# Performance work log

Measured on AMD Instinct MI355X. Metric: run time of the kernel, lower is better.

Reference implementation:

```python
import jax, jax.numpy as jnp
import numpy as np
import math

B, L, C, H = 2, 2048, 768, 12
D = C // H
MAX_SCALE_MUL = math.log(100.0)


def setup_inputs() -> dict:
    key = jax.random.key(0)
    ks = jax.random.split(key, 8)
    std = 0.02
    x = jax.random.normal(ks[0], (B, L, C), dtype=jnp.float32)
    attn_bias = jax.random.normal(ks[1], (1, 1, L, L), dtype=jnp.float32)
    W_qkv = jax.random.normal(ks[2], (3 * C, C), dtype=jnp.float32) * std
    b_qkv = jnp.zeros((3 * C,), dtype=jnp.float32)
    # attn_l2_norm=True: learned per-head log-scale, init log(4)
    scale_mul_log = jnp.full((1, H, 1, 1), math.log(4.0), dtype=jnp.float32)
    W_proj = jax.random.normal(ks[3], (C, C), dtype=jnp.float32) * std
    b_proj = jnp.zeros((C,), dtype=jnp.float32)
    return {"x": x, "attn_bias": attn_bias, "W_qkv": W_qkv, "b_qkv": b_qkv,
            "scale_mul_log": scale_mul_log, "W_proj": W_proj, "b_proj": b_proj}


def _l2norm(t):
    # matches F.normalize(dim=-1, eps=1e-12)
    n = jnp.sqrt(jnp.sum(t * t, axis=-1, keepdims=True))
    return t / jnp.maximum(n, 1e-12)


def reference(x, attn_bias, W_qkv, b_qkv, scale_mul_log, W_proj, b_proj):
    Bx, Lx, Cx = x.shape
    qkv = (x @ W_qkv.T + b_qkv).reshape(Bx, Lx, 3, H, D)
    # -> [3, B, H, L, D]
    qkv = jnp.transpose(qkv, (2, 0, 3, 1, 4))
    q, k, v = qkv[0], qkv[1], qkv[2]
    scale_mul = jnp.exp(jnp.minimum(scale_mul_log, MAX_SCALE_MUL))  # [1,H,1,1]
    q = _l2norm(q) * scale_mul
    k = _l2norm(k)
    # scale = 1 in the l2-norm branch
    attn = jnp.einsum('bhqd,bhkd->bhqk', q, k) + attn_bias
    attn = jax.nn.softmax(attn, axis=-1)
    oup = jnp.einsum('bhqk,bhkd->bhqd', attn, v)          # [B,H,L,D]
    oup = jnp.transpose(oup, (0, 2, 1, 3)).reshape(Bx, Lx, Cx)
    return oup @ W_proj.T + b_proj
```

## Files before the change

kernel.cpp:

```cpp
#include <hip/hip_runtime.h>
#include <math.h>

#define B_ 2
#define L_ 2048
#define C_ 768
#define H_ 12
#define D_ 64
#define M_ (B_ * L_)
#define MAXLOG 4.605170185988091f

typedef __bf16 bf16;
typedef __bf16 bf16x4 __attribute__((ext_vector_type(4)));
typedef __bf16 bf16x8 __attribute__((ext_vector_type(8)));
typedef float  f32x4  __attribute__((ext_vector_type(4)));
typedef short  s16x4  __attribute__((ext_vector_type(4)));

#define SZ_  ((size_t)B_ * H_ * L_ * D_)
#define MC_  ((size_t)M_ * C_)
#define WQ_  ((size_t)3 * C_ * C_)
#define WP_  ((size_t)C_ * C_)

static __device__ __forceinline__ f32x4 mfma16(bf16x4 a, bf16x4 b, f32x4 c) {
#if __has_builtin(__builtin_amdgcn_mfma_f32_16x16x16_bf16)
    return __builtin_amdgcn_mfma_f32_16x16x16_bf16(a, b, c, 0, 0, 0);
#elif __has_builtin(__builtin_amdgcn_mfma_f32_16x16x16bf16_1k)
    return __builtin_amdgcn_mfma_f32_16x16x16bf16_1k(*(s16x4*)&a, *(s16x4*)&b, c, 0, 0, 0);
#else
    f32x4 d;
    asm("v_mfma_f32_16x16x16_bf16 %0, %1, %2, %3" : "=v"(d) : "v"(a), "v"(b), "v"(c));
    return d;
#endif
}

static __device__ __forceinline__ void stage16(const bf16* gsrc, void* ldst) {
#if __has_builtin(__builtin_amdgcn_global_load_lds)
    __builtin_amdgcn_global_load_lds(
        (const __attribute__((address_space(1))) unsigned int*)gsrc,
        (__attribute__((address_space(3))) unsigned int*)ldst, 16, 0, 0);
#else
    *(bf16x8*)ldst = *(const bf16x8*)gsrc;
#endif
}

__global__ __launch_bounds__(256) void prep(
    const float4* __restrict__ x, const float4* __restrict__ Wq,
    const float4* __restrict__ Wp,
    bf16* __restrict__ xb, bf16* __restrict__ wqb,
    bf16* __restrict__ Wh, bf16* __restrict__ Wl)
{
    const int X4 = (int)(MC_ / 4);
    const int W4 = (int)(WQ_ / 4);
    const int S4 = (int)(WP_ / 4);
    const int total = X4 + W4 + S4;

    const int i0 = blockIdx.x * 256 + threadIdx.x;
    const int stride = gridDim.x * 256;
    for (int i = i0; i < total; i += stride) {
        if (i < X4) {
            const float4 v = x[i];
            bf16x4 o; o[0]=(bf16)v.x; o[1]=(bf16)v.y; o[2]=(bf16)v.z; o[3]=(bf16)v.w;
            *(bf16x4*)&xb[(size_t)i * 4] = o;
        } else if (i < X4 + W4) {
            const int j = i - X4;
            const float4 v = Wq[j];
            bf16x4 o; o[0]=(bf16)v.x; o[1]=(bf16)v.y; o[2]=(bf16)v.z; o[3]=(bf16)v.w;
            *(bf16x4*)&wqb[(size_t)j * 4] = o;
        } else {
            const int j = i - X4 - W4;
            const float4 v = Wp[j];
            bf16x4 h, l;
            h[0]=(bf16)v.x; l[0]=(bf16)(v.x-(float)h[0]);
            h[1]=(bf16)v.y; l[1]=(bf16)(v.y-(float)h[1]);
            h[2]=(bf16)v.z; l[2]=(bf16)(v.z-(float)h[2]);
            h[3]=(bf16)v.w; l[3]=(bf16)(v.w-(float)h[3]);
            *(bf16x4*)&Wh[(size_t)j * 4] = h;
            *(bf16x4*)&Wl[(size_t)j * 4] = l;
        }
    }
}

__global__ __launch_bounds__(256) void qkv_mfma(
    const bf16* __restrict__ A, const bf16* __restrict__ W,
    const float* __restrict__ bias, const float* __restrict__ sml,
    bf16* __restrict__ qb, bf16* __restrict__ kb, bf16* __restrict__ vtb)
{
    __shared__ __align__(16) bf16 As[128][64];
    __shared__ __align__(16) bf16 Bs[64][64];

    const int t    = threadIdx.x;
    const int w    = t >> 6;
    const int lane = t & 63;
    const int quad = lane >> 4;
    const int c    = lane & 15;
    const int m0   = blockIdx.x * 128;
    const int n0   = blockIdx.y * 64;

    const int sr = t >> 3;
    const int sc = t & 7;
    const int sx = sc ^ (sr & 7);

    f32x4 acc[2][4];
    #pragma unroll
    for (int mt = 0; mt < 2; ++mt)
        #pragma unroll
        for (int nt = 0; nt < 4; ++nt) acc[mt][nt] = (f32x4){0.f,0.f,0.f,0.f};

    for (int kt = 0; kt < C_; kt += 64) {
        __syncthreads();
        #pragma unroll
        for (int p = 0; p < 4; ++p)
            stage16(&A[(size_t)(m0 + 32 * p + sr) * C_ + kt + 8 * sx],
                    (char*)&As[0][0] + (p * 256 + t) * 16);
        #pragma unroll
        for (int p = 0; p < 2; ++p)
            stage16(&W[(size_t)(n0 + 32 * p + sr) * C_ + kt + 8 * sx],
                    (char*)&Bs[0][0] + (p * 256 + t) * 16);
        __syncthreads();

        #pragma unroll
        for (int ks = 0; ks < 2; ++ks) {
            const int rchunk = ((4 * ks + quad) ^ (c & 7)) * 16;
            #pragma unroll
            for (int mt = 0; mt < 2; ++mt) {
                const bf16x8 a = *(const bf16x8*)((const char*)&As[0][0]
                                 + (size_t)(w * 32 + mt * 16 + c) * 128 + rchunk);
                #pragma unroll
                for (int nt = 0; nt < 4; ++nt) {
                    const bf16x8 b = *(const bf16x8*)((const char*)&Bs[0][0]
                                     + (size_t)(nt * 16 + c) * 128 + rchunk);
                    acc[mt][nt] = __builtin_amdgcn_mfma_f32_16x16x32_bf16(a, b, acc[mt][nt], 0, 0, 0);
                }
            }
        }
    }

    const int three = blockIdx.y / H_;
    const int h     = blockIdx.y % H_;
    const int bidx  = m0 >> 11;
    const int l0    = (m0 & (L_ - 1)) + w * 32;

    if (three < 2) {
        bf16* dst = (three == 0) ? qb : kb;
        const float scale = (three == 0) ? expf(fminf(sml[h], MAXLOG)) : 1.0f;
        #pragma unroll
        for (int mt = 0; mt < 2; ++mt) {
            float val[4][4];
            float ss[4] = {0.f, 0.f, 0.f, 0.f};
            #pragma unroll
            for (int nt = 0; nt < 4; ++nt) {
                const float bb = bias[n0 + nt * 16 + c];
                #pragma unroll
                for (int reg = 0; reg < 4; ++reg) {
                    const float v = acc[mt][nt][reg] + bb;
                    val[nt][reg] = v;
                    ss[reg] += v * v;
                }
            }
            #pragma unroll
            for (int reg = 0; reg < 4; ++reg) {
                float s = ss[reg];
                #pragma unroll
                for (int off = 1; off < 16; off <<= 1) s += __shfl_xor(s, off, 16);
                const float inv = scale / fmaxf(sqrtf(s), 1e-12f);
                const int l = l0 + mt * 16 + quad * 4 + reg;
                #pragma unroll
                for (int nt = 0; nt < 4; ++nt)
                    dst[((size_t)(bidx * H_ + h) * L_ + l) * D_ + nt * 16 + c] =
                        (bf16)(val[nt][reg] * inv);
            }
        }
    } else {
        #pragma unroll
        for (int mt = 0; mt < 2; ++mt)
            #pragma unroll
            for (int nt = 0; nt < 4; ++nt) {
                const int d = nt * 16 + c;
                const float bb = bias[n0 + d];
                const int l = l0 + mt * 16 + quad * 4;
                bf16x4 o;
                #pragma unroll
                for (int reg = 0; reg < 4; ++reg) o[reg] = (bf16)(acc[mt][nt][reg] + bb);
                *(bf16x4*)&vtb[((size_t)(bidx * H_ + h) * D_ + d) * L_ + l] = o;
            }
    }
}

__global__ __launch_bounds__(256, 3) void flash_mfma(
    const bf16* __restrict__ q, const bf16* __restrict__ k,
    const bf16* __restrict__ vt, const float* __restrict__ bias,
    const float* __restrict__ sml,
    bf16* __restrict__ aoh, bf16* __restrict__ aol)
{
    __shared__ __align__(16) bf16 Ks0 [64][72];
    __shared__ __align__(16) bf16 Ks1 [64][72];
    __shared__ __align__(16) bf16 Vts0[64][72];
    __shared__ __align__(16) bf16 Vts1[64][72];

    const int t    = threadIdx.x;
    const int w    = t >> 6;
    const int lane = t & 63;
    const int quad = lane >> 4;
    const int c    = lane & 15;
    const int q0   = blockIdx.x * 64;
    const int bh   = blockIdx.y;
    const int h    = bh % H_;
    const int b    = bh / H_;
    const size_t base  = (size_t)bh * L_ * D_;
    const size_t vbase = (size_t)bh * D_ * L_;
    const int qrow = q0 + w * 16 + c;

    const float FMAX = expf(fminf(sml[h], MAXLOG)) + 8.0f;

    bf16x8 qf[2];
    qf[0] = *(const bf16x8*)&q[base + (size_t)qrow * D_ + quad * 8];
    qf[1] = *(const bf16x8*)&q[base + (size_t)qrow * D_ + 32 + quad * 8];

    const int r0  = t >> 3,         c00 = (t & 7) * 8;
    const int r1  = (t + 256) >> 3, c01 = ((t + 256) & 7) * 8;

    const size_t brow = (size_t)qrow * L_ + 4 * quad;

    float l_acc = 0.f;
    f32x4 o[4];
    #pragma unroll
    for (int dt = 0; dt < 4; ++dt) o[dt] = (f32x4){0.f, 0.f, 0.f, 0.f};

    bf16x8 kreg[2], vreg[2];
    f32x4  bregA[4], bregB[4];

    kreg[0] = *(const bf16x8*)&k [base  + (size_t)r0 * D_ + c00];
    kreg[1] = *(const bf16x8*)&k [base  + (size_t)r1 * D_ + c01];
    vreg[0] = *(const bf16x8*)&vt[vbase + (size_t)r0 * L_ + c00];
    vreg[1] = *(const bf16x8*)&vt[vbase + (size_t)r1 * L_ + c01];
    #pragma unroll
    for (int s = 0; s < 4; ++s)
        bregA[s] = *(const f32x4*)&bias[brow + 16 * s];

    *(bf16x8*)&Ks0 [r0][c00] = kreg[0];
    *(bf16x8*)&Ks0 [r1][c01] = kreg[1];
    *(bf16x8*)&Vts0[r0][c00] = vreg[0];
    *(bf16x8*)&Vts0[r1][c01] = vreg[1];

    kreg[0] = *(const bf16x8*)&k [base  + (size_t)(64 + r0) * D_ + c00];
    kreg[1] = *(const bf16x8*)&k [base  + (size_t)(64 + r1) * D_ + c01];
    vreg[0] = *(const bf16x8*)&vt[vbase + (size_t)r0 * L_ + 64 + c00];
    vreg[1] = *(const bf16x8*)&vt[vbase + (size_t)r1 * L_ + 64 + c01];
    #pragma unroll
    for (int s = 0; s < 4; ++s)
        bregB[s] = *(const f32x4*)&bias[brow + 64 + 16 * s];
    __syncthreads();

#define FSTEP(KS_C, VT_C, KS_N, VT_N, BC, IT) do {                               \
    if ((IT) + 1 < 32) {                                                         \
        *(bf16x8*)&KS_N [r0][c00] = kreg[0];                                     \
        *(bf16x8*)&KS_N [r1][c01] = kreg[1];                                     \
        *(bf16x8*)&VT_N [r0][c00] = vreg[0];                                     \
        *(bf16x8*)&VT_N [r1][c01] = vreg[1];                                     \
    }                                                                            \
    f32x4 st[4];                                                                 \
    _Pragma("unroll") for (int s = 0; s < 4; ++s) st[s] = BC[s];                 \
    if ((IT) + 2 < 32) {                                                         \
        const int kp = ((IT) + 2) * 64;                                          \
        kreg[0] = *(const bf16x8*)&k [base  + (size_t)(kp + r0) * D_ + c00];     \
        kreg[1] = *(const bf16x8*)&k [base  + (size_t)(kp + r1) * D_ + c01];     \
        vreg[0] = *(const bf16x8*)&vt[vbase + (size_t)r0 * L_ + kp + c00];       \
        vreg[1] = *(const bf16x8*)&vt[vbase + (size_t)r1 * L_ + kp + c01];       \
        _Pragma("unroll") for (int s = 0; s < 4; ++s)                            \
            BC[s] = *(const f32x4*)&bias[brow + kp + 16 * s];                    \
    }                                                                            \
    _Pragma("unroll") for (int ks = 0; ks < 2; ++ks)                             \
        _Pragma("unroll") for (int s = 0; s < 4; ++s) {                          \
            const bf16x8 kf = *(const bf16x8*)&KS_C[s*16 + c][ks*32 + quad*8];   \
            st[s] = __builtin_amdgcn_mfma_f32_16x16x32_bf16(kf, qf[ks], st[s], 0, 0, 0); \
        }                                                                        \
    bf16x4 pf[4];                                                                \
    _Pragma("unroll") for (int s = 0; s < 4; ++s)                                \
        _Pragma("unroll") for (int r = 0; r < 4; ++r) {                          \
            const float pv = __expf(st[s][r] - FMAX);                            \
            l_acc += pv;                                                         \
            pf[s][r] = (bf16)pv;                                                 \
        }                                                                        \
    _Pragma("unroll") for (int s = 0; s < 4; ++s)                                \
        _Pragma("unroll") for (int dt = 0; dt < 4; ++dt) {                       \
            const bf16x4 vfr = *(const bf16x4*)&VT_C[dt*16 + c][16*s + 4*quad];  \
            o[dt] = mfma16(vfr, pf[s], o[dt]);                                   \
        }                                                                        \
    __syncthreads();                                                             \
} while (0)

    for (int it = 0; it < 32; it += 2) {
        FSTEP(Ks0, Vts0, Ks1, Vts1, bregA, it);
        FSTEP(Ks1, Vts1, Ks0, Vts0, bregB, it + 1);
    }
#undef FSTEP

    float rs = l_acc;
    rs += __shfl_xor(rs, 16);
    rs += __shfl_xor(rs, 32);
    const float linv = 1.0f / rs;

    const size_t obase = ((size_t)(b * L_ + qrow)) * C_ + h * 64;
    #pragma unroll
    for (int dt = 0; dt < 4; ++dt) {
        bf16x4 hv, lv;
        #pragma unroll
        for (int r = 0; r < 4; ++r) {
            const float v = o[dt][r] * linv;
            hv[r] = (bf16)v;
            lv[r] = (bf16)(v - (float)hv[r]);
        }
        *(bf16x4*)&aoh[obase + dt * 16 + 4 * quad] = hv;
        *(bf16x4*)&aol[obase + dt * 16 + 4 * quad] = lv;
    }
}

__global__ __launch_bounds__(256) void proj_mfma(
    const bf16* __restrict__ Ahg, const bf16* __restrict__ Alg,
    const bf16* __restrict__ Whg, const bf16* __restrict__ Wlg,
    const float* __restrict__ bias, float* __restrict__ outp)
{
    __shared__ __align__(16) bf16 Ah[64][64];
    __shared__ __align__(16) bf16 Al[64][64];
    __shared__ __align__(16) bf16 Bh[64][64];
    __shared__ __align__(16) bf16 Bl[64][64];

    const int t    = threadIdx.x;
    const int w    = t >> 6;
    const int lane = t & 63;
    const int quad = lane >> 4;
    const int c    = lane & 15;
    const int m0   = blockIdx.x * 64;
    const int n0   = blockIdx.y * 64;

    const int sr = t >> 3;
    const int sc = t & 7;
    const int sx = sc ^ (sr & 7);

    f32x4 acc[4];
    #pragma unroll
    for (int nt = 0; nt < 4; ++nt) acc[nt] = (f32x4){0.f,0.f,0.f,0.f};

    for (int kt = 0; kt < C_; kt += 64) {
        __syncthreads();
        #pragma unroll
        for (int p = 0; p < 2; ++p) {
            const size_t ga = (size_t)(m0 + 32 * p + sr) * C_ + kt + 8 * sx;
            const size_t gb = (size_t)(n0 + 32 * p + sr) * C_ + kt + 8 * sx;
            const int    lo = (p * 256 + t) * 16;
            stage16(&Ahg[ga], (char*)&Ah[0][0] + lo);
            stage16(&Alg[ga], (char*)&Al[0][0] + lo);
            stage16(&Whg[gb], (char*)&Bh[0][0] + lo);
            stage16(&Wlg[gb], (char*)&Bl[0][0] + lo);
        }
        __syncthreads();

        #pragma unroll
        for (int ks = 0; ks < 2; ++ks) {
            const int rchunk = ((4 * ks + quad) ^ (c & 7)) * 16;
            const bf16x8 ah = *(const bf16x8*)((const char*)&Ah[0][0]
                              + (size_t)(w * 16 + c) * 128 + rchunk);
            const bf16x8 al = *(const bf16x8*)((const char*)&Al[0][0]
                              + (size_t)(w * 16 + c) * 128 + rchunk);
            #pragma unroll
            for (int nt = 0; nt < 4; ++nt) {
                const bf16x8 bh = *(const bf16x8*)((const char*)&Bh[0][0]
                                  + (size_t)(nt * 16 + c) * 128 + rchunk);
                const bf16x8 bl = *(const bf16x8*)((const char*)&Bl[0][0]
                                  + (size_t)(nt * 16 + c) * 128 + rchunk);
                acc[nt] = __builtin_amdgcn_mfma_f32_16x16x32_bf16(ah, bh, acc[nt], 0, 0, 0);
                acc[nt] = __builtin_amdgcn_mfma_f32_16x16x32_bf16(ah, bl, acc[nt], 0, 0, 0);
                acc[nt] = __builtin_amdgcn_mfma_f32_16x16x32_bf16(al, bh, acc[nt], 0, 0, 0);
            }
        }
    }

    #pragma unroll
    for (int nt = 0; nt < 4; ++nt) {
        const int col = n0 + nt * 16 + c;
        const float bb = bias[col];
        #pragma unroll
        for (int reg = 0; reg < 4; ++reg) {
            const int row = m0 + w * 16 + quad * 4 + reg;
            outp[(size_t)row * C_ + col] = acc[nt][reg] + bb;
        }
    }
}

extern "C" void kernel_launch(void* const* d_in, const int* in_sizes, int n_in,
                              void* d_out, int out_size, void* d_ws, size_t ws_size,
                              hipStream_t stream)
{
    const float* x         = (const float*)d_in[0];
    const float* attn_bias = (const float*)d_in[1];
    const float* W_qkv     = (const float*)d_in[2];
    const float* b_qkv     = (const float*)d_in[3];
    const float* sml       = (const float*)d_in[4];
    const float* W_proj    = (const float*)d_in[5];
    const float* b_proj    = (const float*)d_in[6];
    float* out = (float*)d_out;

    bf16* qb  = (bf16*)d_ws;
    bf16* kb  = qb  + SZ_;
    bf16* vtb = kb  + SZ_;
    bf16* aoh = vtb + SZ_;
    bf16* aol = aoh + MC_;
    bf16* Wh  = aol + MC_;
    bf16* Wl  = Wh  + WP_;
    bf16* xb  = Wl  + WP_;
    bf16* wqb = xb  + MC_;

    prep<<<2048, 256, 0, stream>>>(
        (const float4*)x, (const float4*)W_qkv, (const float4*)W_proj,
        xb, wqb, Wh, Wl);

    qkv_mfma<<<dim3(M_ / 128, (3 * C_) / 64), 256, 0, stream>>>(
        xb, wqb, b_qkv, sml, qb, kb, vtb);

    flash_mfma<<<dim3(L_ / 64, B_ * H_), 256, 0, stream>>>(
        qb, kb, vtb, attn_bias, sml, aoh, aol);

    proj_mfma<<<dim3(M_ / 64, C_ / 64), 256, 0, stream>>>(
        aoh, aol, Wh, Wl, b_proj, out);
}
```

Before: 200.4 us.

## Split flash attention keys across wave pairs with 2x query reuse per wave

Reorganizes the flash attention block so each wave handles 32 query rows (two 16-row tiles sharing each K/V fragment load) and the four waves split the key range into two halves processed in parallel. K/V tiles become 32-key chunks per half, and the partial outputs and row sums of the two key-halves are merged through shared memory at the end. This is meant to halve LDS fragment reads per MFMA and improve MFMA density, at the cost of more accumulator registers, an extra LDS reduction buffer and a final sync.

```diff
diff --git a/kernel.cpp b/kernel.cpp
--- a/kernel.cpp
+++ b/kernel.cpp
@@ -191,126 +191,172 @@
     const float* __restrict__ sml,
     bf16* __restrict__ aoh, bf16* __restrict__ aol)
 {
-    __shared__ __align__(16) bf16 Ks0 [64][72];
-    __shared__ __align__(16) bf16 Ks1 [64][72];
-    __shared__ __align__(16) bf16 Vts0[64][72];
-    __shared__ __align__(16) bf16 Vts1[64][72];
+    __shared__ __align__(16) bf16 Klds[2][2][32][72];
+    __shared__ __align__(16) bf16 Vlds[2][2][64][36];
+    __shared__ __align__(16) float OfT[2][2][4][64][4];
+    __shared__ float lfs[2][2][16];
 
     const int t    = threadIdx.x;
     const int w    = t >> 6;
     const int lane = t & 63;
     const int quad = lane >> 4;
     const int c    = lane & 15;
+    const int wq   = w >> 1;
+    const int wk   = w & 1;
     const int q0   = blockIdx.x * 64;
     const int bh   = blockIdx.y;
     const int h    = bh % H_;
     const int b    = bh / H_;
     const size_t base  = (size_t)bh * L_ * D_;
     const size_t vbase = (size_t)bh * D_ * L_;
-    const int qrow = q0 + w * 16 + c;
+    const int koff = wk << 10;
 
     const float FMAX = expf(fminf(sml[h], MAXLOG)) + 8.0f;
 
-    bf16x8 qf[2];
-    qf[0] = *(const bf16x8*)&q[base + (size_t)qrow * D_ + quad * 8];
-    qf[1] = *(const bf16x8*)&q[base + (size_t)qrow * D_ + 32 + quad * 8];
-
-    const int r0  = t >> 3,         c00 = (t & 7) * 8;
-    const int r1  = (t + 256) >> 3, c01 = ((t + 256) & 7) * 8;
-
-    const size_t brow = (size_t)qrow * L_ + 4 * quad;
-
-    float l_acc = 0.f;
-    f32x4 o[4];
-    #pragma unroll
-    for (int dt = 0; dt < 4; ++dt) o[dt] = (f32x4){0.f, 0.f, 0.f, 0.f};
+    int qrow[2];
+    qrow[0] = q0 + wq * 32 + c;
+    qrow[1] = qrow[0] + 16;
+
+    bf16x8 qf[2][2];
+    #pragma unroll
+    for (int qt = 0; qt < 2; ++qt)
+        #pragma unroll
+        for (int ks = 0; ks < 2; ++ks)
+            qf[qt][ks] = *(const bf16x8*)&q[base + (size_t)qrow[qt] * D_ + ks * 32 + quad * 8];
+
+    const int kr = t >> 3, kc = (t & 7) * 8;
+    const int vr = t >> 2, vc = (t & 3) * 8;
+
+    size_t brow[2];
+    #pragma unroll
+    for (int qt = 0; qt < 2; ++qt)
+        brow[qt] = (size_t)qrow[qt] * L_ + koff + 4 * quad;
+
+    float l_acc[2] = {0.f, 0.f};
+    f32x4 o[2][4];
+    #pragma unroll
+    for (int qt = 0; qt < 2; ++qt)
+        #pragma unroll
+        for (int dt = 0; dt < 4; ++dt) o[qt][dt] = (f32x4){0.f, 0.f, 0.f, 0.f};
 
     bf16x8 kreg[2], vreg[2];
-    f32x4  bregA[4], bregB[4];
-
-    kreg[0] = *(const bf16x8*)&k [base  + (size_t)r0 * D_ + c00];
-    kreg[1] = *(const bf16x8*)&k [base  + (size_t)r1 * D_ + c01];
-    vreg[0] = *(const bf16x8*)&vt[vbase + (size_t)r0 * L_ + c00];
-    vreg[1] = *(const bf16x8*)&vt[vbase + (size_t)r1 * L_ + c01];
-    #pragma unroll
-    for (int s = 0; s < 4; ++s)
-        bregA[s] = *(const f32x4*)&bias[brow + 16 * s];
-
-    *(bf16x8*)&Ks0 [r0][c00] = kreg[0];
-    *(bf16x8*)&Ks0 [r1][c01] = kreg[1];
-    *(bf16x8*)&Vts0[r0][c00] = vreg[0];
-    *(bf16x8*)&Vts0[r1][c01] = vreg[1];
-
-    kreg[0] = *(const bf16x8*)&k [base  + (size_t)(64 + r0) * D_ + c00];
-    kreg[1] = *(const bf16x8*)&k [base  + (size_t)(64 + r1) * D_ + c01];
-    vreg[0] = *(const bf16x8*)&vt[vbase + (size_t)r0 * L_ + 64 + c00];
-    vreg[1] = *(const bf16x8*)&vt[vbase + (size_t)r1 * L_ + 64 + c01];
-    #pragma unroll
-    for (int s = 0; s < 4; ++s)
-        bregB[s] = *(const f32x4*)&bias[brow + 64 + 16 * s];
+    f32x4  bbA[2][2], bbB[2][2];
+
+    #pragma unroll
+    for (int hh = 0; hh < 2; ++hh) {
+        kreg[hh] = *(const bf16x8*)&k [base  + (size_t)(hh * 1024 + kr) * D_ + kc];
+        vreg[hh] = *(const bf16x8*)&vt[vbase + (size_t)vr * L_ + hh * 1024 + vc];
+    }
+    #pragma unroll
+    for (int qt = 0; qt < 2; ++qt)
+        #pragma unroll
+        for (int s = 0; s < 2; ++s) {
+            bbA[qt][s] = *(const f32x4*)&bias[brow[qt] + 16 * s];
+            bbB[qt][s] = *(const f32x4*)&bias[brow[qt] + 32 + 16 * s];
+        }
+    #pragma unroll
+    for (int hh = 0; hh < 2; ++hh) {
+        *(bf16x8*)&Klds[hh][0][kr][kc] = kreg[hh];
+        *(bf16x4*)&Vlds[hh][0][vr][vc]     = __builtin_shufflevector(vreg[hh], vreg[hh], 0,1,2,3);
+        *(bf16x4*)&Vlds[hh][0][vr][vc + 4] = __builtin_shufflevector(vreg[hh], vreg[hh], 4,5,6,7);
+    }
+    #pragma unroll
+    for (int hh = 0; hh < 2; ++hh) {
+        kreg[hh] = *(const bf16x8*)&k [base  + (size_t)(hh * 1024 + 32 + kr) * D_ + kc];
+        vreg[hh] = *(const bf16x8*)&vt[vbase + (size_t)vr * L_ + hh * 1024 + 32 + vc];
+    }
     __syncthreads();
 
-#define FSTEP(KS_C, VT_C, KS_N, VT_N, BC, IT) do {                               \
+#define FSTEP(P, BC, IT) do {                                                    \
     if ((IT) + 1 < 32) {                                                         \
-        *(bf16x8*)&KS_N [r0][c00] = kreg[0];                                     \
-        *(bf16x8*)&KS_N [r1][c01] = kreg[1];                                     \
-        *(bf16x8*)&VT_N [r0][c00] = vreg[0];                                     \
-        *(bf16x8*)&VT_N [r1][c01] = vreg[1];                                     \
+        _Pragma("unroll") for (int hh = 0; hh < 2; ++hh) {                       \
+            *(bf16x8*)&Klds[hh][(P) ^ 1][kr][kc] = kreg[hh];                     \
+            *(bf16x4*)&Vlds[hh][(P) ^ 1][vr][vc]     = __builtin_shufflevector(vreg[hh], vreg[hh], 0,1,2,3); \
+            *(bf16x4*)&Vlds[hh][(P) ^ 1][vr][vc + 4] = __builtin_shufflevector(vreg[hh], vreg[hh], 4,5,6,7); \
+        }                                                                        \
     }                                                                            \
-    f32x4 st[4];                                                                 \
-    _Pragma("unroll") for (int s = 0; s < 4; ++s) st[s] = BC[s];                 \
+    f32x4 st[2][2];                                                              \
+    _Pragma("unroll") for (int qt = 0; qt < 2; ++qt)                             \
+        _Pragma("unroll") for (int s = 0; s < 2; ++s) st[qt][s] = BC[qt][s];     \
     if ((IT) + 2 < 32) {                                                         \
-        const int kp = ((IT) + 2) * 64;                                          \
-        kreg[0] = *(const bf16x8*)&k [base  + (size_t)(kp + r0) * D_ + c00];     \
-        kreg[1] = *(const bf16x8*)&k [base  + (size_t)(kp + r1) * D_ + c01];     \
-        vreg[0] = *(const bf16x8*)&vt[vbase + (size_t)r0 * L_ + kp + c00];       \
-        vreg[1] = *(const bf16x8*)&vt[vbase + (size_t)r1 * L_ + kp + c01];       \
-        _Pragma("unroll") for (int s = 0; s < 4; ++s)                            \
-            BC[s] = *(const f32x4*)&bias[brow + kp + 16 * s];                    \
+        const int kp = ((IT) + 2) * 32;                                          \
+        _Pragma("unroll") for (int hh = 0; hh < 2; ++hh) {                       \
+            kreg[hh] = *(const bf16x8*)&k [base  + (size_t)(hh * 1024 + kp + kr) * D_ + kc]; \
+            vreg[hh] = *(const bf16x8*)&vt[vbase + (size_t)vr * L_ + hh * 1024 + kp + vc];   \
+        }                                                                        \
+        _Pragma("unroll") for (int qt = 0; qt < 2; ++qt)                         \
+            _Pragma("unroll") for (int s = 0; s < 2; ++s)                        \
+                BC[qt][s] = *(const f32x4*)&bias[brow[qt] + kp + 16 * s];        \
     }                                                                            \
     _Pragma("unroll") for (int ks = 0; ks < 2; ++ks)                             \
-        _Pragma("unroll") for (int s = 0; s < 4; ++s) {                          \
-            const bf16x8 kf = *(const bf16x8*)&KS_C[s*16 + c][ks*32 + quad*8];   \
-            st[s] = __builtin_amdgcn_mfma_f32_16x16x32_bf16(kf, qf[ks], st[s], 0, 0, 0); \
+        _Pragma("unroll") for (int s = 0; s < 2; ++s) {                          \
+            const bf16x8 kf = *(const bf16x8*)&Klds[wk][P][s * 16 + c][ks * 32 + quad * 8]; \
+            _Pragma("unroll") for (int qt = 0; qt < 2; ++qt)                     \
+                st[qt][s] = __builtin_amdgcn_mfma_f32_16x16x32_bf16(kf, qf[qt][ks], st[qt][s], 0, 0, 0); \
         }                                                                        \
-    bf16x4 pf[4];                                                                \
-    _Pragma("unroll") for (int s = 0; s < 4; ++s)                                \
-        _Pragma("unroll") for (int r = 0; r < 4; ++r) {                          \
-            const float pv = __expf(st[s][r] - FMAX);                            \
-            l_acc += pv;                                                         \
-            pf[s][r] = (bf16)pv;                                                 \
-        }                                                                        \
-    _Pragma("unroll") for (int s = 0; s < 4; ++s)                                \
+    bf16x4 pf[2][2];                                                             \
+    _Pragma("unroll") for (int qt = 0; qt < 2; ++qt)                             \
+        _Pragma("unroll") for (int s = 0; s < 2; ++s)                            \
+            _Pragma("unroll") for (int r = 0; r < 4; ++r) {                      \
+                const float pv = __expf(st[qt][s][r] - FMAX);                    \
+                l_acc[qt] += pv;                                                 \
+                pf[qt][s][r] = (bf16)pv;                                         \
+            }                                                                    \
+    _Pragma("unroll") for (int s = 0; s < 2; ++s)                                \
         _Pragma("unroll") for (int dt = 0; dt < 4; ++dt) {                       \
-            const bf16x4 vfr = *(const bf16x4*)&VT_C[dt*16 + c][16*s + 4*quad];  \
-            o[dt] = mfma16(vfr, pf[s], o[dt]);                                   \
+            const bf16x4 vfr = *(const bf16x4*)&Vlds[wk][P][dt * 16 + c][16 * s + 4 * quad]; \
+            _Pragma("unroll") for (int qt = 0; qt < 2; ++qt)                     \
+                o[qt][dt] = mfma16(vfr, pf[qt][s], o[qt][dt]);                   \
         }                                                                        \
     __syncthreads();                                                             \
 } while (0)
 
     for (int it = 0; it < 32; it += 2) {
-        FSTEP(Ks0, Vts0, Ks1, Vts1, bregA, it);
-        FSTEP(Ks1, Vts1, Ks0, Vts0, bregB, it + 1);
+        FSTEP(0, bbA, it);
+        FSTEP(1, bbB, it + 1);
     }
 #undef FSTEP
 
-    float rs = l_acc;
-    rs += __shfl_xor(rs, 16);
-    rs += __shfl_xor(rs, 32);
-    const float linv = 1.0f / rs;
-
-    const size_t obase = ((size_t)(b * L_ + qrow)) * C_ + h * 64;
-    #pragma unroll
-    for (int dt = 0; dt < 4; ++dt) {
-        bf16x4 hv, lv;
-        #pragma unroll
-        for (int r = 0; r < 4; ++r) {
-            const float v = o[dt][r] * linv;
-            hv[r] = (bf16)v;
-            lv[r] = (bf16)(v - (float)hv[r]);
-        }
-        *(bf16x4*)&aoh[obase + dt * 16 + 4 * quad] = hv;
-        *(bf16x4*)&aol[obase + dt * 16 + 4 * quad] = lv;
+    float lt[2];
+    #pragma unroll
+    for (int qt = 0; qt < 2; ++qt) {
+        float rs = l_acc[qt];
+        rs += __shfl_xor(rs, 16);
+        rs += __shfl_xor(rs, 32);
+        lt[qt] = rs;
+    }
+
+    if (wk == 1) {
+        #pragma unroll
+        for (int qt = 0; qt < 2; ++qt)
+            #pragma unroll
+            for (int dt = 0; dt < 4; ++dt)
+                *(f32x4*)&OfT[wq][qt][dt][lane][0] = o[qt][dt];
+        if (quad == 0) {
+            lfs[wq][0][c] = lt[0];
+            lfs[wq][1][c] = lt[1];
+        }
+    }
+    __syncthreads();
+    if (wk == 0) {
+        #pragma unroll
+        for (int qt = 0; qt < 2; ++qt) {
+            const float linv = 1.0f / (lt[qt] + lfs[wq][qt][c]);
+            const size_t obase = ((size_t)(b * L_ + qrow[qt])) * C_ + h * 64;
+            #pragma unroll
+            for (int dt = 0; dt < 4; ++dt) {
+                const f32x4 m = *(const f32x4*)&OfT[wq][qt][dt][lane][0];
+                bf16x4 hv, lv;
+                #pragma unroll
+                for (int r = 0; r < 4; ++r) {
+                    const float v = (o[qt][dt][r] + m[r]) * linv;
+                    hv[r] = (bf16)v;
+                    lv[r] = (bf16)(v - (float)hv[r]);
+                }
+                *(bf16x4*)&aoh[obase + dt * 16 + 4 * quad] = hv;
+                *(bf16x4*)&aol[obase + dt * 16 + 4 * quad] = lv;
+            }
+        }
     }
 }
 
```

Result: slower. 235.9 us (+17.7%).

## Shrink flash attention tiles to 32 queries and 32 keys per block

Applied to the files above, without the earlier changes.

The flash kernel now runs with 128 threads (2 waves) per block covering 32 query rows, and streams K/V in 32-key chunks over 64 iterations instead of 64-key chunks over 32. LDS buffers shrink accordingly and the grid doubles to 1536 blocks. The goal is more blocks for better CU occupancy and load balance. The cost is twice as many barriers and loop iterations, and each K/V tile loaded to LDS is reused by fewer query rows.

```diff
diff --git a/kernel.cpp b/kernel.cpp
--- a/kernel.cpp
+++ b/kernel.cpp
@@ -185,23 +185,21 @@
     }
 }
 
-__global__ __launch_bounds__(256, 3) void flash_mfma(
+__global__ __launch_bounds__(128, 3) void flash_mfma(
     const bf16* __restrict__ q, const bf16* __restrict__ k,
     const bf16* __restrict__ vt, const float* __restrict__ bias,
     const float* __restrict__ sml,
     bf16* __restrict__ aoh, bf16* __restrict__ aol)
 {
-    __shared__ __align__(16) bf16 Ks0 [64][72];
-    __shared__ __align__(16) bf16 Ks1 [64][72];
-    __shared__ __align__(16) bf16 Vts0[64][72];
-    __shared__ __align__(16) bf16 Vts1[64][72];
+    __shared__ __align__(16) bf16 Klds[2][32][72];
+    __shared__ __align__(16) bf16 Vlds[2][64][36];
 
     const int t    = threadIdx.x;
     const int w    = t >> 6;
     const int lane = t & 63;
     const int quad = lane >> 4;
     const int c    = lane & 15;
-    const int q0   = blockIdx.x * 64;
+    const int q0   = blockIdx.x * 32;
     const int bh   = blockIdx.y;
     const int h    = bh % H_;
     const int b    = bh / H_;
@@ -215,8 +213,8 @@
     qf[0] = *(const bf16x8*)&q[base + (size_t)qrow * D_ + quad * 8];
     qf[1] = *(const bf16x8*)&q[base + (size_t)qrow * D_ + 32 + quad * 8];
 
-    const int r0  = t >> 3,         c00 = (t & 7) * 8;
-    const int r1  = (t + 256) >> 3, c01 = ((t + 256) & 7) * 8;
+    const int kr = t >> 3, kc = (t & 7) * 8;
+    const int vr = t >> 2, vc = (t & 3) * 8;
 
     const size_t brow = (size_t)qrow * L_ + 4 * quad;
 
@@ -226,71 +224,71 @@
     for (int dt = 0; dt < 4; ++dt) o[dt] = (f32x4){0.f, 0.f, 0.f, 0.f};
 
     bf16x8 kreg[2], vreg[2];
-    f32x4  bregA[4], bregB[4];
-
-    kreg[0] = *(const bf16x8*)&k [base  + (size_t)r0 * D_ + c00];
-    kreg[1] = *(const bf16x8*)&k [base  + (size_t)r1 * D_ + c01];
-    vreg[0] = *(const bf16x8*)&vt[vbase + (size_t)r0 * L_ + c00];
-    vreg[1] = *(const bf16x8*)&vt[vbase + (size_t)r1 * L_ + c01];
-    #pragma unroll
-    for (int s = 0; s < 4; ++s)
-        bregA[s] = *(const f32x4*)&bias[brow + 16 * s];
-
-    *(bf16x8*)&Ks0 [r0][c00] = kreg[0];
-    *(bf16x8*)&Ks0 [r1][c01] = kreg[1];
-    *(bf16x8*)&Vts0[r0][c00] = vreg[0];
-    *(bf16x8*)&Vts0[r1][c01] = vreg[1];
-
-    kreg[0] = *(const bf16x8*)&k [base  + (size_t)(64 + r0) * D_ + c00];
-    kreg[1] = *(const bf16x8*)&k [base  + (size_t)(64 + r1) * D_ + c01];
-    vreg[0] = *(const bf16x8*)&vt[vbase + (size_t)r0 * L_ + 64 + c00];
-    vreg[1] = *(const bf16x8*)&vt[vbase + (size_t)r1 * L_ + 64 + c01];
-    #pragma unroll
-    for (int s = 0; s < 4; ++s)
-        bregB[s] = *(const f32x4*)&bias[brow + 64 + 16 * s];
+    f32x4  bbA[2], bbB[2];
+
+    #pragma unroll
+    for (int j = 0; j < 2; ++j) {
+        kreg[j] = *(const bf16x8*)&k [base  + (size_t)(16 * j + kr) * D_ + kc];
+        vreg[j] = *(const bf16x8*)&vt[vbase + (size_t)(32 * j + vr) * L_ + vc];
+    }
+    #pragma unroll
+    for (int s = 0; s < 2; ++s) {
+        bbA[s] = *(const f32x4*)&bias[brow + 16 * s];
+        bbB[s] = *(const f32x4*)&bias[brow + 32 + 16 * s];
+    }
+    #pragma unroll
+    for (int j = 0; j < 2; ++j) {
+        *(bf16x8*)&Klds[0][16 * j + kr][kc] = kreg[j];
+        *(bf16x8*)&Vlds[0][32 * j + vr][vc] = vreg[j];
+    }
+    #pragma unroll
+    for (int j = 0; j < 2; ++j) {
+        kreg[j] = *(const bf16x8*)&k [base  + (size_t)(32 + 16 * j + kr) * D_ + kc];
+        vreg[j] = *(const bf16x8*)&vt[vbase + (size_t)(32 * j + vr) * L_ + 32 + vc];
+    }
     __syncthreads();
 
-#define FSTEP(KS_C, VT_C, KS_N, VT_N, BC, IT) do {                               \
-    if ((IT) + 1 < 32) {                                                         \
-        *(bf16x8*)&KS_N [r0][c00] = kreg[0];                                     \
-        *(bf16x8*)&KS_N [r1][c01] = kreg[1];                                     \
-        *(bf16x8*)&VT_N [r0][c00] = vreg[0];                                     \
-        *(bf16x8*)&VT_N [r1][c01] = vreg[1];                                     \
+#define FSTEP(P, BC, IT) do {                                                    \
+    if ((IT) + 1 < 64) {                                                         \
+        _Pragma("unroll") for (int j = 0; j < 2; ++j) {                          \
+            *(bf16x8*)&Klds[(P) ^ 1][16 * j + kr][kc] = kreg[j];                 \
+            *(bf16x8*)&Vlds[(P) ^ 1][32 * j + vr][vc] = vreg[j];                 \
+        }                                                                        \
     }                                                                            \
-    f32x4 st[4];                                                                 \
-    _Pragma("unroll") for (int s = 0; s < 4; ++s) st[s] = BC[s];                 \
-    if ((IT) + 2 < 32) {                                                         \
-        const int kp = ((IT) + 2) * 64;                                          \
-        kreg[0] = *(const bf16x8*)&k [base  + (size_t)(kp + r0) * D_ + c00];     \
-        kreg[1] = *(const bf16x8*)&k [base  + (size_t)(kp + r1) * D_ + c01];     \
-        vreg[0] = *(const bf16x8*)&vt[vbase + (size_t)r0 * L_ + kp + c00];       \
-        vreg[1] = *(const bf16x8*)&vt[vbase + (size_t)r1 * L_ + kp + c01];       \
-        _Pragma("unroll") for (int s = 0; s < 4; ++s)                            \
+    f32x4 st[2];                                                                 \
+    _Pragma("unroll") for (int s = 0; s < 2; ++s) st[s] = BC[s];                 \
+    if ((IT) + 2 < 64) {                                                         \
+        const int kp = ((IT) + 2) * 32;                                          \
+        _Pragma("unroll") for (int j = 0; j < 2; ++j) {                          \
+            kreg[j] = *(const bf16x8*)&k [base  + (size_t)(kp + 16 * j + kr) * D_ + kc]; \
+            vreg[j] = *(const bf16x8*)&vt[vbase + (size_t)(32 * j + vr) * L_ + kp + vc]; \
+        }                                                                        \
+        _Pragma("unroll") for (int s = 0; s < 2; ++s)                            \
             BC[s] = *(const f32x4*)&bias[brow + kp + 16 * s];                    \
     }                                                                            \
     _Pragma("unroll") for (int ks = 0; ks < 2; ++ks)                             \
-        _Pragma("unroll") for (int s = 0; s < 4; ++s) {                          \
-            const bf16x8 kf = *(const bf16x8*)&KS_C[s*16 + c][ks*32 + quad*8];   \
+        _Pragma("unroll") for (int s = 0; s < 2; ++s) {                          \
+            const bf16x8 kf = *(const bf16x8*)&Klds[P][s * 16 + c][ks * 32 + quad * 8]; \
             st[s] = __builtin_amdgcn_mfma_f32_16x16x32_bf16(kf, qf[ks], st[s], 0, 0, 0); \
         }                                                                        \
-    bf16x4 pf[4];                                                                \
-    _Pragma("unroll") for (int s = 0; s < 4; ++s)                                \
+    bf16x4 pf[2];                                                                \
+    _Pragma("unroll") for (int s = 0; s < 2; ++s)                                \
         _Pragma("unroll") for (int r = 0; r < 4; ++r) {                          \
             const float pv = __expf(st[s][r] - FMAX);                            \
             l_acc += pv;                                                         \
             pf[s][r] = (bf16)pv;                                                 \
         }                                                                        \
-    _Pragma("unroll") for (int s = 0; s < 4; ++s)                                \
+    _Pragma("unroll") for (int s = 0; s < 2; ++s)                                \
         _Pragma("unroll") for (int dt = 0; dt < 4; ++dt) {                       \
-            const bf16x4 vfr = *(const bf16x4*)&VT_C[dt*16 + c][16*s + 4*quad];  \
+            const bf16x4 vfr = *(const bf16x4*)&Vlds[P][dt * 16 + c][16 * s + 4 * quad]; \
             o[dt] = mfma16(vfr, pf[s], o[dt]);                                   \
         }                                                                        \
     __syncthreads();                                                             \
 } while (0)
 
-    for (int it = 0; it < 32; it += 2) {
-        FSTEP(Ks0, Vts0, Ks1, Vts1, bregA, it);
-        FSTEP(Ks1, Vts1, Ks0, Vts0, bregB, it + 1);
+    for (int it = 0; it < 64; it += 2) {
+        FSTEP(0, bbA, it);
+        FSTEP(1, bbB, it + 1);
     }
 #undef FSTEP
 
@@ -416,7 +414,7 @@
     qkv_mfma<<<dim3(M_ / 128, (3 * C_) / 64), 256, 0, stream>>>(
         xb, wqb, b_qkv, sml, qb, kb, vtb);
 
-    flash_mfma<<<dim3(L_ / 64, B_ * H_), 256, 0, stream>>>(
+    flash_mfma<<<dim3(L_ / 32, B_ * H_), 128, 0, stream>>>(
         qb, kb, vtb, attn_bias, sml, aoh, aol);
 
     proj_mfma<<<dim3(M_ / 64, C_ / 64), 256, 0, stream>>>(
```

Measured after the change: 206.9 us. 1.03x slower.
